# Kernel optimization log

Measured on AMD Instinct MI355X. Metric: run time of the kernel, lower is better.

Reference implementation:

```python
import jax, jax.numpy as jnp
import numpy as np

DIM = 512
NUM_HEADS = 16
WS = 8  # window_size
N = WS * WS
B = 1024


def get_relative_index(h, w):
    coords_h = np.arange(h)[:, None].repeat(w, axis=1)
    coords_w = np.arange(w)[None, :].repeat(h, axis=0)
    coords = np.stack([coords_h, coords_w], axis=-1).reshape(-1, 2)  # [N,2]
    rel = coords[:, None, :] - coords[None, :, :]
    rel = rel + np.array([h - 1, w - 1])
    rel[:, :, 0] *= 2 * w - 1
    return rel.sum(-1).astype(np.int32)  # [N,N]


def setup_inputs() -> dict:
    key = jax.random.key(0)
    ks = jax.random.split(key, 6)
    table_size = (2 * WS - 1) * (2 * WS - 1)  # 225
    return {
        "x": jax.random.normal(ks[0], (B, N, DIM), dtype=jnp.float32),
        "qkv_weight": jax.random.normal(ks[1], (3 * DIM, DIM), dtype=jnp.float32) * 0.02,
        "qkv_bias": jax.random.normal(ks[2], (3 * DIM,), dtype=jnp.float32) * 0.02,
        "proj_weight": jax.random.normal(ks[3], (DIM, DIM), dtype=jnp.float32) * 0.02,
        "proj_bias": jax.random.normal(ks[4], (DIM,), dtype=jnp.float32) * 0.02,
        "relative_table": jax.random.normal(ks[5], (table_size, 2 * NUM_HEADS), dtype=jnp.float32) * 0.02,
        "relative_index": jnp.asarray(get_relative_index(WS, WS)),
    }


def reference(x, qkv_weight, qkv_bias, proj_weight, proj_bias, relative_table, relative_index):
    B_, n, C = x.shape
    H = NUM_HEADS
    hd = C // H
    scale = hd ** -0.5
    # qkv projection: [B,N,3C] -> [3,B,H,N,hd]
    qkv = (x @ qkv_weight.T + qkv_bias).reshape(B_, n, 3, H, hd).transpose(2, 0, 3, 1, 4)
    q, k, v = qkv[0], qkv[1], qkv[2]
    attn = jnp.einsum("bhnd,bhmd->bhnm", q * scale, k)  # [B,H,N,N]
    # learned relative-position bias + post-softmax scale
    params = relative_table[relative_index.reshape(-1)].reshape(n, n, 2 * H)
    params = params.transpose(2, 0, 1)  # [2H,N,N]
    rel_bias, rel_scale = params[:H], params[H:]
    attn = jax.nn.softmax(attn + rel_bias[None], axis=-1)
    attn = attn * rel_scale[None]
    out = jnp.einsum("bhnm,bhmd->bhnd", attn, v)
    out = out.transpose(0, 2, 1, 3).reshape(B_, n, C)
    return out @ proj_weight.T + proj_bias
```

## Files before the change

kernel.cpp:

```cpp
#include <hip/hip_runtime.h>

typedef unsigned short u16;
typedef unsigned int   u32;
typedef __attribute__((ext_vector_type(8))) short bf16x8;
typedef __attribute__((ext_vector_type(4))) float f32x4;

#define SCALE 0.17677669529663687f

__device__ __forceinline__ u16 f2bf(float f){
  u32 x = __float_as_uint(f);
  x += 0x7fffu + ((x >> 16) & 1u);
  return (u16)(x >> 16);
}
__device__ __forceinline__ float bf2f(u16 u){
  return __uint_as_float(((u32)u) << 16);
}


__global__ void prep_kernel(const float* __restrict__ qkvw, const float* __restrict__ projw,
                            const float* __restrict__ table, const int* __restrict__ relidx,
                            u16* __restrict__ qkvw_b, u16* __restrict__ projw_b,
                            u16* __restrict__ biasT, u16* __restrict__ scaleT){
  int i = blockIdx.x * 256 + threadIdx.x;
  if (i < 786432) {
    qkvw_b[i] = f2bf(qkvw[i]);
  } else if (i < 1048576) {
    int j = i - 786432; projw_b[j] = f2bf(projw[j]);
  } else if (i < 1114112) {
    int j = i - 1048576; int h = j >> 12, rc = j & 4095;
    int idx = relidx[rc];
    int row = rc >> 6, col = rc & 63;
    int noff = h*4096 + row*64 + (col & 15)*4 + (col >> 4);
    biasT [noff] = f2bf(table[idx*32 + h]);
    scaleT[noff] = f2bf(table[idx*32 + 16 + h]);
  }
}

__global__ void xconv_kernel(const float* __restrict__ x, u16* __restrict__ xb){
  size_t i = (size_t)blockIdx.x * 256 + threadIdx.x;
  const float4* xp = (const float4*)x;
  float4 a = xp[2*i], b = xp[2*i+1];
  union { u16 u[8]; uint4 v; } o;
  o.u[0]=f2bf(a.x); o.u[1]=f2bf(a.y); o.u[2]=f2bf(a.z); o.u[3]=f2bf(a.w);
  o.u[4]=f2bf(b.x); o.u[5]=f2bf(b.y); o.u[6]=f2bf(b.z); o.u[7]=f2bf(b.w);
  *(uint4*)(xb + 8*i) = o.v;
}

__global__ __launch_bounds__(512, 2) void gemm_qkv_kernel(
    const u16* __restrict__ A, const u16* __restrict__ W,
    const float* __restrict__ bias, u16* __restrict__ outp)
{
  __shared__ u16 lds[3][16384];
  const int tid = threadIdx.x, lane = tid & 63, wid = tid >> 6;
  const int wave_base = tid & ~63;

  const int cpx = gridDim.x >> 3;
  const int bid = (blockIdx.x & 7) * cpx + (blockIdx.x >> 3);
  const int mt = bid / 6, nt = bid % 6;
  const size_t m0 = (size_t)mt * 256;
  const int n0 = nt * 256;
  const int wm = wid >> 2, wn = wid & 3;

  const f32x4 z = {0.f, 0.f, 0.f, 0.f};
  f32x4 acc[8][4];
#pragma unroll
  for (int i = 0; i < 8; i++)
#pragma unroll
    for (int j = 0; j < 4; j++) acc[i][j] = z;

  auto stageA = [&](int ch){
    const int slot = ch % 3;
    const int kb = ch * 32;
#pragma unroll
    for (int c = 0; c < 2; ++c){
      const int t = c*512 + tid;
      const int row = t >> 2, sl = t & 3;
      const int lsl = sl ^ ((row >> 1) & 3);
      const u16* ga = A + (m0 + row)*512 + kb + lsl*8;
      u16* la = &lds[slot][(size_t)(c*512 + wave_base)*8];
      __builtin_amdgcn_global_load_lds((const __attribute__((address_space(1))) u32*)ga,
                                       (__attribute__((address_space(3))) u32*)la, 16, 0, 0);
    }
  };
  auto stageB = [&](int ch){
    const int slot = ch % 3;
    const int kb = ch * 32;
#pragma unroll
    for (int c = 0; c < 2; ++c){
      const int t = c*512 + tid;
      const int col = t >> 2, sl = t & 3;
      const int lsl = sl ^ ((col >> 1) & 3);
      const u16* gb = W + (size_t)(n0 + col)*512 + kb + lsl*8;
      u16* lb = &lds[slot][8192 + (size_t)(c*512 + wave_base)*8];
      __builtin_amdgcn_global_load_lds((const __attribute__((address_space(1))) u32*)gb,
                                       (__attribute__((address_space(3))) u32*)lb, 16, 0, 0);
    }
  };

  stageA(0); stageB(0);
  stageA(1); stageB(1);
  asm volatile("s_waitcnt vmcnt(4)" ::: "memory");
  __builtin_amdgcn_s_barrier();

  const int lq = lane & 15, lk = lane >> 4;
#pragma unroll
  for (int ch = 0; ch < 16; ++ch){
    const int slot = ch % 3;
    const u16* As = &lds[slot][0];
    const u16* Bs = &lds[slot][8192];
    bf16x8 af[4], bfr[4], af2[4];

#pragma unroll
    for (int i = 0; i < 4; ++i){
      const int row = wm*128 + i*16 + lq;
      af[i]  = *(const bf16x8*)&As[row*32 + (lk ^ ((row >> 1) & 3))*8];
      const int col = wn*64 + i*16 + lq;
      bfr[i] = *(const bf16x8*)&Bs[col*32 + (lk ^ ((col >> 1) & 3))*8];
    }
    if (ch + 2 < 16) stageA(ch + 2);
    __builtin_amdgcn_s_barrier();
    asm volatile("s_waitcnt lgkmcnt(0)" ::: "memory");
    __builtin_amdgcn_sched_barrier(0);
    __builtin_amdgcn_s_setprio(1);
#pragma unroll
    for (int i = 0; i < 4; ++i)
#pragma unroll
      for (int j = 0; j < 4; ++j)
        acc[i][j] = __builtin_amdgcn_mfma_f32_16x16x32_bf16(af[i], bfr[j], acc[i][j], 0, 0, 0);
    __builtin_amdgcn_s_setprio(0);
    __builtin_amdgcn_s_barrier();

#pragma unroll
    for (int i = 0; i < 4; ++i){
      const int row = wm*128 + 64 + i*16 + lq;
      af2[i] = *(const bf16x8*)&As[row*32 + (lk ^ ((row >> 1) & 3))*8];
    }
    if (ch + 2 < 16) stageB(ch + 2);
    __builtin_amdgcn_s_barrier();
    asm volatile("s_waitcnt lgkmcnt(0)" ::: "memory");
    __builtin_amdgcn_sched_barrier(0);
    __builtin_amdgcn_s_setprio(1);
#pragma unroll
    for (int i = 0; i < 4; ++i)
#pragma unroll
      for (int j = 0; j < 4; ++j)
        acc[4+i][j] = __builtin_amdgcn_mfma_f32_16x16x32_bf16(af2[i], bfr[j], acc[4+i][j], 0, 0, 0);
    __builtin_amdgcn_s_setprio(0);
    if (ch < 14)       { asm volatile("s_waitcnt vmcnt(4)" ::: "memory"); }
    else if (ch == 14) { asm volatile("s_waitcnt vmcnt(0)" ::: "memory"); }
    if (ch < 15) __builtin_amdgcn_s_barrier();
  }

  const int lr = (lane >> 4) << 2;
  const int lc = lane & 15;
  u16* o = outp;
  float bv[4], sc[4];
#pragma unroll
  for (int nf = 0; nf < 4; ++nf){
    const int col = n0 + wn*64 + nf*16 + lc;
    bv[nf] = bias[col];
    sc[nf] = (col < 512) ? SCALE : 1.f;
  }
#pragma unroll
  for (int mf = 0; mf < 8; ++mf){
#pragma unroll
    for (int r = 0; r < 4; ++r){
      const size_t row = m0 + wm*128 + mf*16 + lr + r;
#pragma unroll
      for (int nf = 0; nf < 4; ++nf){
        const int col = n0 + wn*64 + nf*16 + lc;
        o[row*1536 + col] = f2bf((acc[mf][nf][r] + bv[nf]) * sc[nf]);
      }
    }
  }
}

__global__ __launch_bounds__(512) void attnproj_kernel(
    const u16* __restrict__ qkv, const u16* __restrict__ biasT,
    const u16* __restrict__ scaleT, const u16* __restrict__ projw,
    const float* __restrict__ projb, float* __restrict__ out)
{
  __shared__ u16 lds[62464];
  const int tid = threadIdx.x, lane = tid & 63, wid = tid >> 6;
  const int lq = lane & 15, lg = lane >> 4;
  const int b = blockIdx.x;
  const u16* qb = qkv + (size_t)b * 64 * 1536;
  u16* vs = &lds[32768 + wid*3712];
  u16* Ps = vs + 2560;
  const f32x4 z = {0.f, 0.f, 0.f, 0.f};

#pragma unroll
  for (int hh = 0; hh < 2; ++hh){
    const int h = wid*2 + hh;
    asm volatile("s_waitcnt lgkmcnt(0)" ::: "memory");
    __builtin_amdgcn_sched_barrier(0);
#pragma unroll
    for (int c = 0; c < 4; ++c){
      const int u = c*64 + lane, row = u >> 2, sg = u & 3;
      uint4 t = *(const uint4*)(qb + row*1536 + 1024 + h*32 + sg*8);
      *(uint4*)&vs[row*40 + sg*8] = t;
    }
    bf16x8 qf[4], kf[4];
#pragma unroll
    for (int i = 0; i < 4; ++i){
      qf[i] = *(const bf16x8*)(qb + (i*16+lq)*1536 + h*32 + lg*8);
      kf[i] = *(const bf16x8*)(qb + (i*16+lq)*1536 + 512 + h*32 + lg*8);
    }
    f32x4 s[4][4];
#pragma unroll
    for (int i = 0; i < 4; ++i)
#pragma unroll
      for (int j = 0; j < 4; ++j)
        s[i][j] = __builtin_amdgcn_mfma_f32_16x16x32_bf16(qf[i], kf[j], z, 0, 0, 0);

    const u16* bT = biasT + h*4096;
    const u16* sT = scaleT + h*4096;
    f32x4 o[4][2];
#pragma unroll
    for (int i = 0; i < 4; ++i){ o[i][0] = z; o[i][1] = z; }

#pragma unroll
    for (int i = 0; i < 4; ++i){
#pragma unroll
      for (int r = 0; r < 4; ++r){
        const int row = i*16 + lg*4 + r;
        const ushort4 b4 = *(const ushort4*)&bT[row*64 + lq*4];
        const ushort4 s4 = *(const ushort4*)&sT[row*64 + lq*4];
        float vals[4];
        vals[0] = s[i][0][r] + bf2f(b4.x);
        vals[1] = s[i][1][r] + bf2f(b4.y);
        vals[2] = s[i][2][r] + bf2f(b4.z);
        vals[3] = s[i][3][r] + bf2f(b4.w);
        float mx = fmaxf(fmaxf(vals[0], vals[1]), fmaxf(vals[2], vals[3]));
        mx = fmaxf(mx, __shfl_xor(mx, 1));
        mx = fmaxf(mx, __shfl_xor(mx, 2));
        mx = fmaxf(mx, __shfl_xor(mx, 4));
        mx = fmaxf(mx, __shfl_xor(mx, 8));
        float sm = 0.f;
#pragma unroll
        for (int j = 0; j < 4; ++j){ vals[j] = __expf(vals[j] - mx); sm += vals[j]; }
        sm += __shfl_xor(sm, 1);
        sm += __shfl_xor(sm, 2);
        sm += __shfl_xor(sm, 4);
        sm += __shfl_xor(sm, 8);
        const float inv = 1.f / sm;
        const u16 sv[4] = {s4.x, s4.y, s4.z, s4.w};
#pragma unroll
        for (int j = 0; j < 4; ++j)
          Ps[(lg*4 + r)*72 + j*16 + lq] = f2bf(vals[j] * inv * bf2f(sv[j]));
      }
      asm volatile("s_waitcnt lgkmcnt(0)" ::: "memory");
      __builtin_amdgcn_sched_barrier(0);
#pragma unroll
      for (int kc = 0; kc < 2; ++kc){
        bf16x8 pa = *(const bf16x8*)&Ps[lq*72 + kc*32 + lg*8];
#pragma unroll
        for (int c2 = 0; c2 < 2; ++c2){
          union { u16 u[8]; bf16x8 v; } vf;
#pragma unroll
          for (int e = 0; e < 8; ++e)
            vf.u[e] = vs[(kc*32 + lg*8 + e)*40 + c2*16 + lq];
          o[i][c2] = __builtin_amdgcn_mfma_f32_16x16x32_bf16(pa, vf.v, o[i][c2], 0, 0, 0);
        }
      }
    }
#pragma unroll
    for (int i = 0; i < 4; ++i){
#pragma unroll
      for (int c2 = 0; c2 < 2; ++c2){
#pragma unroll
        for (int r = 0; r < 4; ++r){
          const int row = i*16 + lg*4 + r;
          const int c = h*32 + c2*16 + lq;
          const int phys = (c >> 3) ^ (row & 7);
          lds[row*512 + phys*8 + (c & 7)] = f2bf(o[i][c2][r]);
        }
      }
    }
  }
  __syncthreads();

  const int n0 = wid * 64;
  f32x4 pacc[4][4];
#pragma unroll
  for (int i = 0; i < 4; i++)
#pragma unroll
    for (int j = 0; j < 4; j++) pacc[i][j] = z;

#pragma unroll
  for (int ch = 0; ch < 16; ++ch){
    bf16x8 oa[4], wb[4];
#pragma unroll
    for (int mi = 0; mi < 4; ++mi){
      const int row = mi*16 + lq;
      const int phys = (ch*4 + lg) ^ (lq & 7);
      oa[mi] = *(const bf16x8*)&lds[row*512 + phys*8];
    }
#pragma unroll
    for (int nj = 0; nj < 4; ++nj)
      wb[nj] = *(const bf16x8*)(projw + (size_t)(n0 + nj*16 + lq)*512 + ch*32 + lg*8);
#pragma unroll
    for (int mi = 0; mi < 4; ++mi)
#pragma unroll
      for (int nj = 0; nj < 4; ++nj)
        pacc[mi][nj] = __builtin_amdgcn_mfma_f32_16x16x32_bf16(oa[mi], wb[nj], pacc[mi][nj], 0, 0, 0);
  }

  float bv[4];
#pragma unroll
  for (int nj = 0; nj < 4; ++nj) bv[nj] = projb[n0 + nj*16 + lq];
#pragma unroll
  for (int mi = 0; mi < 4; ++mi){
#pragma unroll
    for (int r = 0; r < 4; ++r){
      const size_t grow = (size_t)b*64 + mi*16 + lg*4 + r;
#pragma unroll
      for (int nj = 0; nj < 4; ++nj)
        out[grow*512 + n0 + nj*16 + lq] = pacc[mi][nj][r] + bv[nj];
    }
  }
}

extern "C" void kernel_launch(void* const* d_in, const int* in_sizes, int n_in,
                              void* d_out, int out_size, void* d_ws, size_t ws_size,
                              hipStream_t stream)
{
  const float* x      = (const float*)d_in[0];
  const float* qkvw   = (const float*)d_in[1];
  const float* qkvb   = (const float*)d_in[2];
  const float* projw  = (const float*)d_in[3];
  const float* projb  = (const float*)d_in[4];
  const float* table  = (const float*)d_in[5];
  const int*   relidx = (const int*)d_in[6];
  char* ws = (char*)d_ws;

  u16* qkvw_b = (u16*)(ws + 0);
  u16* projw_b= (u16*)(ws + 1572864);
  u16* biasT  = (u16*)(ws + 2097152);
  u16* scaleT = (u16*)(ws + 2228224);
  u16* qkvws  = (u16*)(ws + 2359296);
  u16* xb     = (u16*)(ws + 203685888);

  if (ws_size < 270794752ull) return;

  prep_kernel<<<dim3(4352), dim3(256), 0, stream>>>(qkvw, projw, table, relidx,
                                                    qkvw_b, projw_b, biasT, scaleT);
  xconv_kernel<<<dim3(16384), dim3(256), 0, stream>>>(x, xb);
  gemm_qkv_kernel<<<dim3(1536), dim3(512), 0, stream>>>(xb, qkvw_b, qkvb, qkvws);
  attnproj_kernel<<<dim3(1024), dim3(512), 0, stream>>>(qkvws, biasT, scaleT,
                                                        projw_b, projb, (float*)d_out);
}
```

Measured before the change: 344.9 us.

## Split fused attention+proj into head-major attention kernel and pipelined proj GEMM

The QKV GEMM epilogue now writes Q/K/V in a per-(batch, head) contiguous layout, so the attention kernel reads each head's 64x32 tiles contiguously. Attention runs as a separate kernel with one wave per (batch, head) and a swizzled V buffer in LDS. The output projection becomes its own LDS-pipelined GEMM with global_load_lds triple buffering. This replaces the fused per-batch kernel whose projection streamed weights directly from global memory. The cost is an extra bf16 round trip of the attention output through memory and one more kernel launch.

```diff
diff --git a/kernel.cpp b/kernel.cpp
--- a/kernel.cpp
+++ b/kernel.cpp
@@ -154,169 +154,228 @@
   const int lr = (lane >> 4) << 2;
   const int lc = lane & 15;
   u16* o = outp;
-  float bv[4], sc[4];
+  float bv[4], sc[4]; int pb[4];
 #pragma unroll
   for (int nf = 0; nf < 4; ++nf){
     const int col = n0 + wn*64 + nf*16 + lc;
     bv[nf] = bias[col];
     sc[nf] = (col < 512) ? SCALE : 1.f;
+    const int which = col >> 9, h = (col >> 5) & 15, d = col & 31;
+    pb[nf] = (h*3 + which)*2048 + d;
   }
 #pragma unroll
   for (int mf = 0; mf < 8; ++mf){
 #pragma unroll
     for (int r = 0; r < 4; ++r){
-      const size_t row = m0 + wm*128 + mf*16 + lr + r;
+      const int row = (int)m0 + wm*128 + mf*16 + lr + r;
+      const size_t base = (size_t)(row >> 6) * 98304 + (row & 63)*32;
+#pragma unroll
+      for (int nf = 0; nf < 4; ++nf)
+        o[base + pb[nf]] = f2bf((acc[mf][nf][r] + bv[nf]) * sc[nf]);
+    }
+  }
+}
+
+__global__ __launch_bounds__(512) void attn_kernel(
+    const u16* __restrict__ qkv, const u16* __restrict__ biasT,
+    const u16* __restrict__ scaleT, u16* __restrict__ attn_out)
+{
+  __shared__ u16 lds[8][3200];
+  const int tid = threadIdx.x, lane = tid & 63, wid = tid >> 6;
+  const int lq = lane & 15, lg = lane >> 4;
+  const int bh = blockIdx.x * 8 + wid;
+  const int b = bh >> 4, h = bh & 15;
+  const u16* qb = qkv + (size_t)bh * 6144;
+  u16* vs = &lds[wid][0];
+  u16* Ps = &lds[wid][2048];
+  const f32x4 z = {0.f, 0.f, 0.f, 0.f};
+
+#pragma unroll
+  for (int c = 0; c < 4; ++c){
+    const int u = c*64 + lane, row = u >> 2, sl = u & 3;
+    uint4 t = *(const uint4*)(qb + 4096 + row*32 + sl*8);
+    *(uint4*)&vs[row*32 + (sl ^ ((row >> 3) & 3))*8] = t;
+  }
+  bf16x8 kf[4];
+#pragma unroll
+  for (int i = 0; i < 4; ++i)
+    kf[i] = *(const bf16x8*)(qb + 2048 + (i*16 + lq)*32 + lg*8);
+
+  f32x4 o[4][2];
+#pragma unroll
+  for (int i = 0; i < 4; ++i){ o[i][0] = z; o[i][1] = z; }
+
+  const u16* bT = biasT + h*4096;
+  const u16* sT = scaleT + h*4096;
+
+  asm volatile("s_waitcnt lgkmcnt(0)" ::: "memory");
+  __builtin_amdgcn_sched_barrier(0);
+
+#pragma unroll
+  for (int i = 0; i < 4; ++i){
+    bf16x8 qf = *(const bf16x8*)(qb + (i*16 + lq)*32 + lg*8);
+    f32x4 s[4];
+#pragma unroll
+    for (int j = 0; j < 4; ++j)
+      s[j] = __builtin_amdgcn_mfma_f32_16x16x32_bf16(qf, kf[j], z, 0, 0, 0);
+
+#pragma unroll
+    for (int r = 0; r < 4; ++r){
+      const int row = i*16 + lg*4 + r;
+      const ushort4 b4 = *(const ushort4*)&bT[row*64 + lq*4];
+      const ushort4 s4 = *(const ushort4*)&sT[row*64 + lq*4];
+      float vals[4];
+      vals[0] = s[0][r] + bf2f(b4.x);
+      vals[1] = s[1][r] + bf2f(b4.y);
+      vals[2] = s[2][r] + bf2f(b4.z);
+      vals[3] = s[3][r] + bf2f(b4.w);
+      float mx = fmaxf(fmaxf(vals[0], vals[1]), fmaxf(vals[2], vals[3]));
+      mx = fmaxf(mx, __shfl_xor(mx, 1));
+      mx = fmaxf(mx, __shfl_xor(mx, 2));
+      mx = fmaxf(mx, __shfl_xor(mx, 4));
+      mx = fmaxf(mx, __shfl_xor(mx, 8));
+      float sm = 0.f;
+#pragma unroll
+      for (int j = 0; j < 4; ++j){ vals[j] = __expf(vals[j] - mx); sm += vals[j]; }
+      sm += __shfl_xor(sm, 1);
+      sm += __shfl_xor(sm, 2);
+      sm += __shfl_xor(sm, 4);
+      sm += __shfl_xor(sm, 8);
+      const float inv = 1.f / sm;
+      const u16 sv[4] = {s4.x, s4.y, s4.z, s4.w};
+#pragma unroll
+      for (int j = 0; j < 4; ++j)
+        Ps[(lg*4 + r)*72 + j*16 + lq] = f2bf(vals[j] * inv * bf2f(sv[j]));
+    }
+    asm volatile("s_waitcnt lgkmcnt(0)" ::: "memory");
+    __builtin_amdgcn_sched_barrier(0);
+#pragma unroll
+    for (int kc = 0; kc < 2; ++kc){
+      bf16x8 pa = *(const bf16x8*)&Ps[lq*72 + kc*32 + lg*8];
+#pragma unroll
+      for (int c2 = 0; c2 < 2; ++c2){
+        union { u16 u[8]; bf16x8 v; } vf;
+#pragma unroll
+        for (int e = 0; e < 8; ++e){
+          const int rv = kc*32 + lg*8 + e;
+          const int d = c2*16 + lq;
+          vf.u[e] = vs[rv*32 + ((d >> 3) ^ ((rv >> 3) & 3))*8 + (d & 7)];
+        }
+        o[i][c2] = __builtin_amdgcn_mfma_f32_16x16x32_bf16(pa, vf.v, o[i][c2], 0, 0, 0);
+      }
+    }
+    asm volatile("s_waitcnt lgkmcnt(0)" ::: "memory");
+    __builtin_amdgcn_sched_barrier(0);
+  }
+
+#pragma unroll
+  for (int i = 0; i < 4; ++i){
+#pragma unroll
+    for (int c2 = 0; c2 < 2; ++c2){
+#pragma unroll
+      for (int r = 0; r < 4; ++r){
+        const int n = i*16 + lg*4 + r;
+        attn_out[((size_t)b*64 + n)*512 + h*32 + c2*16 + lq] = f2bf(o[i][c2][r]);
+      }
+    }
+  }
+}
+
+__global__ __launch_bounds__(512, 4) void gemm_proj_kernel(
+    const u16* __restrict__ A, const u16* __restrict__ W,
+    const float* __restrict__ bias, float* __restrict__ outp)
+{
+  __shared__ u16 lds[3][12288];
+  const int tid = threadIdx.x, lane = tid & 63;
+  const int wid = tid >> 6, wave_base = tid & ~63;
+
+  const int cpx = gridDim.x >> 3;
+  const int bid = (blockIdx.x & 7) * cpx + (blockIdx.x >> 3);
+  const int mt = bid >> 1, nt = bid & 1;
+  const size_t m0 = (size_t)mt * 128;
+  const int n0 = nt * 256;
+  const int wm = wid >> 2, wn = wid & 3;
+
+  const f32x4 z = {0.f, 0.f, 0.f, 0.f};
+  f32x4 acc[4][4];
+#pragma unroll
+  for (int i = 0; i < 4; i++)
+#pragma unroll
+    for (int j = 0; j < 4; j++) acc[i][j] = z;
+
+  auto stage = [&](int ch){
+    const int slot = ch % 3;
+    const int kb = ch * 32;
+    {
+      const int row = tid >> 2, sl = tid & 3;
+      const int lsl = sl ^ ((row >> 1) & 3);
+      const u16* ga = A + (m0 + row)*512 + kb + lsl*8;
+      u16* la = &lds[slot][(size_t)wave_base*8];
+      __builtin_amdgcn_global_load_lds((const __attribute__((address_space(1))) u32*)ga,
+                                       (__attribute__((address_space(3))) u32*)la, 16, 0, 0);
+    }
+#pragma unroll
+    for (int c = 0; c < 2; ++c){
+      const int t = c*512 + tid;
+      const int col = t >> 2, sl = t & 3;
+      const int lsl = sl ^ ((col >> 1) & 3);
+      const u16* gb = W + (size_t)(n0 + col)*512 + kb + lsl*8;
+      u16* lb = &lds[slot][4096 + (size_t)(c*512 + wave_base)*8];
+      __builtin_amdgcn_global_load_lds((const __attribute__((address_space(1))) u32*)gb,
+                                       (__attribute__((address_space(3))) u32*)lb, 16, 0, 0);
+    }
+  };
+
+  stage(0);
+  stage(1);
+  asm volatile("s_waitcnt vmcnt(3)" ::: "memory");
+  __builtin_amdgcn_s_barrier();
+
+  const int lq = lane & 15, lk = lane >> 4;
+#pragma unroll
+  for (int ch = 0; ch < 16; ++ch){
+    const int slot = ch % 3;
+    if (ch + 2 < 16) stage(ch + 2);
+    const u16* As = &lds[slot][0];
+    const u16* Bs = &lds[slot][4096];
+    bf16x8 af[4], bfr[4];
+#pragma unroll
+    for (int i = 0; i < 4; ++i){
+      const int row = wm*64 + i*16 + lq;
+      af[i]  = *(const bf16x8*)&As[row*32 + (lk ^ ((row >> 1) & 3))*8];
+      const int col = wn*64 + i*16 + lq;
+      bfr[i] = *(const bf16x8*)&Bs[col*32 + (lk ^ ((col >> 1) & 3))*8];
+    }
+    asm volatile("s_waitcnt lgkmcnt(0)" ::: "memory");
+    __builtin_amdgcn_sched_barrier(0);
+    __builtin_amdgcn_s_setprio(1);
+#pragma unroll
+    for (int i = 0; i < 4; ++i)
+#pragma unroll
+      for (int j = 0; j < 4; ++j)
+        acc[i][j] = __builtin_amdgcn_mfma_f32_16x16x32_bf16(af[i], bfr[j], acc[i][j], 0, 0, 0);
+    __builtin_amdgcn_s_setprio(0);
+    if (ch <= 13)      { asm volatile("s_waitcnt vmcnt(3)" ::: "memory"); }
+    else if (ch == 14) { asm volatile("s_waitcnt vmcnt(0)" ::: "memory"); }
+    if (ch < 15) __builtin_amdgcn_s_barrier();
+  }
+
+  const int lr = (lane >> 4) << 2;
+  const int lc = lane & 15;
+  float bv[4];
+#pragma unroll
+  for (int nf = 0; nf < 4; ++nf)
+    bv[nf] = bias[n0 + wn*64 + nf*16 + lc];
+#pragma unroll
+  for (int mf = 0; mf < 4; ++mf){
+#pragma unroll
+    for (int r = 0; r < 4; ++r){
+      const size_t row = m0 + wm*64 + mf*16 + lr + r;
 #pragma unroll
       for (int nf = 0; nf < 4; ++nf){
         const int col = n0 + wn*64 + nf*16 + lc;
-        o[row*1536 + col] = f2bf((acc[mf][nf][r] + bv[nf]) * sc[nf]);
+        outp[row*512 + col] = acc[mf][nf][r] + bv[nf];
       }
-    }
-  }
-}
-
-__global__ __launch_bounds__(512) void attnproj_kernel(
-    const u16* __restrict__ qkv, const u16* __restrict__ biasT,
-    const u16* __restrict__ scaleT, const u16* __restrict__ projw,
-    const float* __restrict__ projb, float* __restrict__ out)
-{
-  __shared__ u16 lds[62464];
-  const int tid = threadIdx.x, lane = tid & 63, wid = tid >> 6;
-  const int lq = lane & 15, lg = lane >> 4;
-  const int b = blockIdx.x;
-  const u16* qb = qkv + (size_t)b * 64 * 1536;
-  u16* vs = &lds[32768 + wid*3712];
-  u16* Ps = vs + 2560;
-  const f32x4 z = {0.f, 0.f, 0.f, 0.f};
-
-#pragma unroll
-  for (int hh = 0; hh < 2; ++hh){
-    const int h = wid*2 + hh;
-    asm volatile("s_waitcnt lgkmcnt(0)" ::: "memory");
-    __builtin_amdgcn_sched_barrier(0);
-#pragma unroll
-    for (int c = 0; c < 4; ++c){
-      const int u = c*64 + lane, row = u >> 2, sg = u & 3;
-      uint4 t = *(const uint4*)(qb + row*1536 + 1024 + h*32 + sg*8);
-      *(uint4*)&vs[row*40 + sg*8] = t;
-    }
-    bf16x8 qf[4], kf[4];
-#pragma unroll
-    for (int i = 0; i < 4; ++i){
-      qf[i] = *(const bf16x8*)(qb + (i*16+lq)*1536 + h*32 + lg*8);
-      kf[i] = *(const bf16x8*)(qb + (i*16+lq)*1536 + 512 + h*32 + lg*8);
-    }
-    f32x4 s[4][4];
-#pragma unroll
-    for (int i = 0; i < 4; ++i)
-#pragma unroll
-      for (int j = 0; j < 4; ++j)
-        s[i][j] = __builtin_amdgcn_mfma_f32_16x16x32_bf16(qf[i], kf[j], z, 0, 0, 0);
-
-    const u16* bT = biasT + h*4096;
-    const u16* sT = scaleT + h*4096;
-    f32x4 o[4][2];
-#pragma unroll
-    for (int i = 0; i < 4; ++i){ o[i][0] = z; o[i][1] = z; }
-
-#pragma unroll
-    for (int i = 0; i < 4; ++i){
-#pragma unroll
-      for (int r = 0; r < 4; ++r){
-        const int row = i*16 + lg*4 + r;
-        const ushort4 b4 = *(const ushort4*)&bT[row*64 + lq*4];
-        const ushort4 s4 = *(const ushort4*)&sT[row*64 + lq*4];
-        float vals[4];
-        vals[0] = s[i][0][r] + bf2f(b4.x);
-        vals[1] = s[i][1][r] + bf2f(b4.y);
-        vals[2] = s[i][2][r] + bf2f(b4.z);
-        vals[3] = s[i][3][r] + bf2f(b4.w);
-        float mx = fmaxf(fmaxf(vals[0], vals[1]), fmaxf(vals[2], vals[3]));
-        mx = fmaxf(mx, __shfl_xor(mx, 1));
-        mx = fmaxf(mx, __shfl_xor(mx, 2));
-        mx = fmaxf(mx, __shfl_xor(mx, 4));
-        mx = fmaxf(mx, __shfl_xor(mx, 8));
-        float sm = 0.f;
-#pragma unroll
-        for (int j = 0; j < 4; ++j){ vals[j] = __expf(vals[j] - mx); sm += vals[j]; }
-        sm += __shfl_xor(sm, 1);
-        sm += __shfl_xor(sm, 2);
-        sm += __shfl_xor(sm, 4);
-        sm += __shfl_xor(sm, 8);
-        const float inv = 1.f / sm;
-        const u16 sv[4] = {s4.x, s4.y, s4.z, s4.w};
-#pragma unroll
-        for (int j = 0; j < 4; ++j)
-          Ps[(lg*4 + r)*72 + j*16 + lq] = f2bf(vals[j] * inv * bf2f(sv[j]));
-      }
-      asm volatile("s_waitcnt lgkmcnt(0)" ::: "memory");
-      __builtin_amdgcn_sched_barrier(0);
-#pragma unroll
-      for (int kc = 0; kc < 2; ++kc){
-        bf16x8 pa = *(const bf16x8*)&Ps[lq*72 + kc*32 + lg*8];
-#pragma unroll
-        for (int c2 = 0; c2 < 2; ++c2){
-          union { u16 u[8]; bf16x8 v; } vf;
-#pragma unroll
-          for (int e = 0; e < 8; ++e)
-            vf.u[e] = vs[(kc*32 + lg*8 + e)*40 + c2*16 + lq];
-          o[i][c2] = __builtin_amdgcn_mfma_f32_16x16x32_bf16(pa, vf.v, o[i][c2], 0, 0, 0);
-        }
-      }
-    }
-#pragma unroll
-    for (int i = 0; i < 4; ++i){
-#pragma unroll
-      for (int c2 = 0; c2 < 2; ++c2){
-#pragma unroll
-        for (int r = 0; r < 4; ++r){
-          const int row = i*16 + lg*4 + r;
-          const int c = h*32 + c2*16 + lq;
-          const int phys = (c >> 3) ^ (row & 7);
-          lds[row*512 + phys*8 + (c & 7)] = f2bf(o[i][c2][r]);
-        }
-      }
-    }
-  }
-  __syncthreads();
-
-  const int n0 = wid * 64;
-  f32x4 pacc[4][4];
-#pragma unroll
-  for (int i = 0; i < 4; i++)
-#pragma unroll
-    for (int j = 0; j < 4; j++) pacc[i][j] = z;
-
-#pragma unroll
-  for (int ch = 0; ch < 16; ++ch){
-    bf16x8 oa[4], wb[4];
-#pragma unroll
-    for (int mi = 0; mi < 4; ++mi){
-      const int row = mi*16 + lq;
-      const int phys = (ch*4 + lg) ^ (lq & 7);
-      oa[mi] = *(const bf16x8*)&lds[row*512 + phys*8];
-    }
-#pragma unroll
-    for (int nj = 0; nj < 4; ++nj)
-      wb[nj] = *(const bf16x8*)(projw + (size_t)(n0 + nj*16 + lq)*512 + ch*32 + lg*8);
-#pragma unroll
-    for (int mi = 0; mi < 4; ++mi)
-#pragma unroll
-      for (int nj = 0; nj < 4; ++nj)
-        pacc[mi][nj] = __builtin_amdgcn_mfma_f32_16x16x32_bf16(oa[mi], wb[nj], pacc[mi][nj], 0, 0, 0);
-  }
-
-  float bv[4];
-#pragma unroll
-  for (int nj = 0; nj < 4; ++nj) bv[nj] = projb[n0 + nj*16 + lq];
-#pragma unroll
-  for (int mi = 0; mi < 4; ++mi){
-#pragma unroll
-    for (int r = 0; r < 4; ++r){
-      const size_t grow = (size_t)b*64 + mi*16 + lg*4 + r;
-#pragma unroll
-      for (int nj = 0; nj < 4; ++nj)
-        out[grow*512 + n0 + nj*16 + lq] = pacc[mi][nj][r] + bv[nj];
     }
   }
 }
@@ -338,15 +397,16 @@
   u16* projw_b= (u16*)(ws + 1572864);
   u16* biasT  = (u16*)(ws + 2097152);
   u16* scaleT = (u16*)(ws + 2228224);
-  u16* qkvws  = (u16*)(ws + 2359296);
+  u16* qkvs   = (u16*)(ws + 2359296);
   u16* xb     = (u16*)(ws + 203685888);
+  u16* attn_o = xb;
 
   if (ws_size < 270794752ull) return;
 
   prep_kernel<<<dim3(4352), dim3(256), 0, stream>>>(qkvw, projw, table, relidx,
                                                     qkvw_b, projw_b, biasT, scaleT);
   xconv_kernel<<<dim3(16384), dim3(256), 0, stream>>>(x, xb);
-  gemm_qkv_kernel<<<dim3(1536), dim3(512), 0, stream>>>(xb, qkvw_b, qkvb, qkvws);
-  attnproj_kernel<<<dim3(1024), dim3(512), 0, stream>>>(qkvws, biasT, scaleT,
-                                                        projw_b, projb, (float*)d_out);
-}
+  gemm_qkv_kernel<<<dim3(1536), dim3(512), 0, stream>>>(xb, qkvw_b, qkvb, qkvs);
+  attn_kernel<<<dim3(2048), dim3(512), 0, stream>>>(qkvs, biasT, scaleT, attn_o);
+  gemm_proj_kernel<<<dim3(1024), dim3(512), 0, stream>>>(attn_o, projw_b, projb, (float*)d_out);
+}
```

After: 291.9 us. 15.4% less time.

## Store QKV head-major and pre-tile projection weights for contiguous attention loads

Applied to the files above, without the earlier changes.

The QKV GEMM epilogue now writes q, k and v per (batch, head) as contiguous 64x32 tiles. Each head's loads in the attention kernel therefore become dense 64-byte rows instead of strided 3 KB rows. The projection weight is repacked in the prep kernel into a fragment-ordered layout, so each lane's MFMA operand load is fully contiguous. The V tile in LDS uses an XOR swizzle in place of padding, which shrinks scratch memory. The Q fragment and S scores are also computed per 16-row block to lower register pressure. In exchange, the GEMM epilogue writes become scattered, which may cost store efficiency.

```diff
diff --git a/kernel.cpp b/kernel.cpp
--- a/kernel.cpp
+++ b/kernel.cpp
@@ -19,13 +19,16 @@
 
 __global__ void prep_kernel(const float* __restrict__ qkvw, const float* __restrict__ projw,
                             const float* __restrict__ table, const int* __restrict__ relidx,
-                            u16* __restrict__ qkvw_b, u16* __restrict__ projw_b,
+                            u16* __restrict__ qkvw_b, u16* __restrict__ Wp,
                             u16* __restrict__ biasT, u16* __restrict__ scaleT){
   int i = blockIdx.x * 256 + threadIdx.x;
   if (i < 786432) {
     qkvw_b[i] = f2bf(qkvw[i]);
   } else if (i < 1048576) {
-    int j = i - 786432; projw_b[j] = f2bf(projw[j]);
+    int j = i - 786432;
+    const int e  = j & 7, lg = (j >> 3) & 3, lq = (j >> 5) & 15;
+    const int ch = (j >> 9) & 15, ct = j >> 13;
+    Wp[j] = f2bf(projw[(ct*16 + lq)*512 + ch*32 + lg*8 + e]);
   } else if (i < 1114112) {
     int j = i - 1048576; int h = j >> 12, rc = j & 4095;
     int idx = relidx[rc];
@@ -154,83 +157,87 @@
   const int lr = (lane >> 4) << 2;
   const int lc = lane & 15;
   u16* o = outp;
-  float bv[4], sc[4];
+  float bv[4], sc[4]; int pb[4];
 #pragma unroll
   for (int nf = 0; nf < 4; ++nf){
     const int col = n0 + wn*64 + nf*16 + lc;
     bv[nf] = bias[col];
     sc[nf] = (col < 512) ? SCALE : 1.f;
+    const int which = col >> 9, h = (col >> 5) & 15, d = col & 31;
+    pb[nf] = (h*3 + which)*2048 + d;
   }
 #pragma unroll
   for (int mf = 0; mf < 8; ++mf){
 #pragma unroll
     for (int r = 0; r < 4; ++r){
-      const size_t row = m0 + wm*128 + mf*16 + lr + r;
-#pragma unroll
-      for (int nf = 0; nf < 4; ++nf){
-        const int col = n0 + wn*64 + nf*16 + lc;
-        o[row*1536 + col] = f2bf((acc[mf][nf][r] + bv[nf]) * sc[nf]);
-      }
+      const int row = (int)m0 + wm*128 + mf*16 + lr + r;
+      const size_t base = (size_t)(row >> 6) * 98304 + (row & 63)*32;
+#pragma unroll
+      for (int nf = 0; nf < 4; ++nf)
+        o[base + pb[nf]] = f2bf((acc[mf][nf][r] + bv[nf]) * sc[nf]);
     }
   }
 }
 
 __global__ __launch_bounds__(512) void attnproj_kernel(
     const u16* __restrict__ qkv, const u16* __restrict__ biasT,
-    const u16* __restrict__ scaleT, const u16* __restrict__ projw,
+    const u16* __restrict__ scaleT, const u16* __restrict__ Wp,
     const float* __restrict__ projb, float* __restrict__ out)
 {
-  __shared__ u16 lds[62464];
+  __shared__ u16 O[32768];
+  __shared__ u16 scratch[8][3200];
   const int tid = threadIdx.x, lane = tid & 63, wid = tid >> 6;
   const int lq = lane & 15, lg = lane >> 4;
   const int b = blockIdx.x;
-  const u16* qb = qkv + (size_t)b * 64 * 1536;
-  u16* vs = &lds[32768 + wid*3712];
-  u16* Ps = vs + 2560;
+  u16* vs = &scratch[wid][0];
+  u16* Ps = &scratch[wid][2048];
   const f32x4 z = {0.f, 0.f, 0.f, 0.f};
 
 #pragma unroll
   for (int hh = 0; hh < 2; ++hh){
     const int h = wid*2 + hh;
+    const u16* qb = qkv + ((size_t)b*16 + h) * 6144;
     asm volatile("s_waitcnt lgkmcnt(0)" ::: "memory");
     __builtin_amdgcn_sched_barrier(0);
 #pragma unroll
     for (int c = 0; c < 4; ++c){
-      const int u = c*64 + lane, row = u >> 2, sg = u & 3;
-      uint4 t = *(const uint4*)(qb + row*1536 + 1024 + h*32 + sg*8);
-      *(uint4*)&vs[row*40 + sg*8] = t;
-    }
-    bf16x8 qf[4], kf[4];
-#pragma unroll
-    for (int i = 0; i < 4; ++i){
-      qf[i] = *(const bf16x8*)(qb + (i*16+lq)*1536 + h*32 + lg*8);
-      kf[i] = *(const bf16x8*)(qb + (i*16+lq)*1536 + 512 + h*32 + lg*8);
-    }
-    f32x4 s[4][4];
+      const int u = c*64 + lane, row = u >> 2, sl = u & 3;
+      uint4 t = *(const uint4*)(qb + 4096 + row*32 + sl*8);
+      *(uint4*)&vs[row*32 + (sl ^ ((row >> 3) & 3))*8] = t;
+    }
+    bf16x8 kf[4];
 #pragma unroll
     for (int i = 0; i < 4; ++i)
-#pragma unroll
-      for (int j = 0; j < 4; ++j)
-        s[i][j] = __builtin_amdgcn_mfma_f32_16x16x32_bf16(qf[i], kf[j], z, 0, 0, 0);
+      kf[i] = *(const bf16x8*)(qb + 2048 + (i*16 + lq)*32 + lg*8);
+
+    f32x4 o[4][2];
+#pragma unroll
+    for (int i = 0; i < 4; ++i){ o[i][0] = z; o[i][1] = z; }
 
     const u16* bT = biasT + h*4096;
     const u16* sT = scaleT + h*4096;
-    f32x4 o[4][2];
-#pragma unroll
-    for (int i = 0; i < 4; ++i){ o[i][0] = z; o[i][1] = z; }
+
+    asm volatile("s_waitcnt lgkmcnt(0)" ::: "memory");
+    __builtin_amdgcn_sched_barrier(0);
 
 #pragma unroll
     for (int i = 0; i < 4; ++i){
+      bf16x8 qf = *(const bf16x8*)(qb + (i*16 + lq)*32 + lg*8);
+      f32x4 s[4];
+#pragma unroll
+      for (int j = 0; j < 4; ++j)
+        s[j] = __builtin_amdgcn_mfma_f32_16x16x32_bf16(qf, kf[j], z, 0, 0, 0);
+
 #pragma unroll
       for (int r = 0; r < 4; ++r){
         const int row = i*16 + lg*4 + r;
         const ushort4 b4 = *(const ushort4*)&bT[row*64 + lq*4];
         const ushort4 s4 = *(const ushort4*)&sT[row*64 + lq*4];
         float vals[4];
-        vals[0] = s[i][0][r] + bf2f(b4.x);
-        vals[1] = s[i][1][r] + bf2f(b4.y);
-        vals[2] = s[i][2][r] + bf2f(b4.z);
-        vals[3] = s[i][3][r] + bf2f(b4.w);
+        vals[0] = s[0][r] + bf2f(b4.x);
+        vals[1] = s[1][r] + bf2f(b4.y);
+        vals[2] = s[2][r] + bf2f(b4.z);
+        vals[3] = s[3][r] + bf2f(b4.w);
         float mx = fmaxf(fmaxf(vals[0], vals[1]), fmaxf(vals[2], vals[3]));
         mx = fmaxf(mx, __shfl_xor(mx, 1));
         mx = fmaxf(mx, __shfl_xor(mx, 2));
@@ -258,11 +265,16 @@
         for (int c2 = 0; c2 < 2; ++c2){
           union { u16 u[8]; bf16x8 v; } vf;
 #pragma unroll
-          for (int e = 0; e < 8; ++e)
-            vf.u[e] = vs[(kc*32 + lg*8 + e)*40 + c2*16 + lq];
+          for (int e = 0; e < 8; ++e){
+            const int rv = kc*32 + lg*8 + e;
+            const int d = c2*16 + lq;
+            vf.u[e] = vs[rv*32 + ((d >> 3) ^ ((rv >> 3) & 3))*8 + (d & 7)];
+          }
           o[i][c2] = __builtin_amdgcn_mfma_f32_16x16x32_bf16(pa, vf.v, o[i][c2], 0, 0, 0);
         }
       }
+      asm volatile("s_waitcnt lgkmcnt(0)" ::: "memory");
+      __builtin_amdgcn_sched_barrier(0);
     }
 #pragma unroll
     for (int i = 0; i < 4; ++i){
@@ -273,32 +285,34 @@
           const int row = i*16 + lg*4 + r;
           const int c = h*32 + c2*16 + lq;
           const int phys = (c >> 3) ^ (row & 7);
-          lds[row*512 + phys*8 + (c & 7)] = f2bf(o[i][c2][r]);
+          O[row*512 + phys*8 + (c & 7)] = f2bf(o[i][c2][r]);
         }
       }
     }
   }
   __syncthreads();
 
-  const int n0 = wid * 64;
   f32x4 pacc[4][4];
 #pragma unroll
   for (int i = 0; i < 4; i++)
 #pragma unroll
     for (int j = 0; j < 4; j++) pacc[i][j] = z;
 
+  const int laneoff = (lq*4 + lg)*8;
 #pragma unroll
   for (int ch = 0; ch < 16; ++ch){
     bf16x8 oa[4], wb[4];
+#pragma unroll
+    for (int nj = 0; nj < 4; ++nj){
+      const int ct = wid*4 + nj;
+      wb[nj] = *(const bf16x8*)(Wp + (ct*16 + ch)*512 + laneoff);
+    }
 #pragma unroll
     for (int mi = 0; mi < 4; ++mi){
       const int row = mi*16 + lq;
       const int phys = (ch*4 + lg) ^ (lq & 7);
-      oa[mi] = *(const bf16x8*)&lds[row*512 + phys*8];
-    }
-#pragma unroll
-    for (int nj = 0; nj < 4; ++nj)
-      wb[nj] = *(const bf16x8*)(projw + (size_t)(n0 + nj*16 + lq)*512 + ch*32 + lg*8);
+      oa[mi] = *(const bf16x8*)&O[row*512 + phys*8];
+    }
 #pragma unroll
     for (int mi = 0; mi < 4; ++mi)
 #pragma unroll
@@ -306,6 +320,7 @@
         pacc[mi][nj] = __builtin_amdgcn_mfma_f32_16x16x32_bf16(oa[mi], wb[nj], pacc[mi][nj], 0, 0, 0);
   }
 
+  const int n0 = wid * 64;
   float bv[4];
 #pragma unroll
   for (int nj = 0; nj < 4; ++nj) bv[nj] = projb[n0 + nj*16 + lq];
@@ -335,18 +350,18 @@
   char* ws = (char*)d_ws;
 
   u16* qkvw_b = (u16*)(ws + 0);
-  u16* projw_b= (u16*)(ws + 1572864);
+  u16* Wp     = (u16*)(ws + 1572864);
   u16* biasT  = (u16*)(ws + 2097152);
   u16* scaleT = (u16*)(ws + 2228224);
-  u16* qkvws  = (u16*)(ws + 2359296);
+  u16* qkvs   = (u16*)(ws + 2359296);
   u16* xb     = (u16*)(ws + 203685888);
 
   if (ws_size < 270794752ull) return;
 
   prep_kernel<<<dim3(4352), dim3(256), 0, stream>>>(qkvw, projw, table, relidx,
-                                                    qkvw_b, projw_b, biasT, scaleT);
+                                                    qkvw_b, Wp, biasT, scaleT);
   xconv_kernel<<<dim3(16384), dim3(256), 0, stream>>>(x, xb);
-  gemm_qkv_kernel<<<dim3(1536), dim3(512), 0, stream>>>(xb, qkvw_b, qkvb, qkvws);
-  attnproj_kernel<<<dim3(1024), dim3(512), 0, stream>>>(qkvws, biasT, scaleT,
-                                                        projw_b, projb, (float*)d_out);
-}
+  gemm_qkv_kernel<<<dim3(1536), dim3(512), 0, stream>>>(xb, qkvw_b, qkvb, qkvs);
+  attnproj_kernel<<<dim3(1024), dim3(512), 0, stream>>>(qkvs, biasT, scaleT,
+                                                        Wp, projb, (float*)d_out);
+}
```

Measured after the change: 306.3 us. 11.2% less time.
